# Kernel tuning notes

Measured on AMD Instinct MI355X. Metric: run time of the kernel, lower is better.

Reference implementation:

```python
import jax, jax.numpy as jnp
import numpy as np

B, C, H, W = 2, 64, 96, 96
CI = C // 2  # inter_channels


def _conv1x1(x, w, b):
    # x: (B,C,H,W), w: (O,C), b: (O,) -> (B,O,H,W)
    return jnp.einsum('bchw,oc->bohw', x, w) + b[None, :, None, None]


def setup_inputs() -> dict:
    key = jax.random.key(0)
    ks = jax.random.split(key, 9)
    s_in = 1.0 / np.sqrt(C)
    s_ci = 1.0 / np.sqrt(CI)
    return {
        'x': jax.random.normal(ks[0], (B, C, H, W), jnp.float32),
        'theta_w': jax.random.uniform(ks[1], (CI, C), jnp.float32, -s_in, s_in),
        'theta_b': jax.random.uniform(ks[2], (CI,), jnp.float32, -s_in, s_in),
        'phi_w': jax.random.uniform(ks[3], (CI, C), jnp.float32, -s_in, s_in),
        'phi_b': jax.random.uniform(ks[4], (CI,), jnp.float32, -s_in, s_in),
        'g_w': jax.random.uniform(ks[5], (CI, C), jnp.float32, -s_in, s_in),
        'g_b': jax.random.uniform(ks[6], (CI,), jnp.float32, -s_in, s_in),
        'rec_w': jax.random.uniform(ks[7], (C, CI), jnp.float32, -s_ci, s_ci),
        'rec_b': jax.random.uniform(ks[8], (C,), jnp.float32, -s_ci, s_ci),
    }


def reference(x, theta_w, theta_b, phi_w, phi_b, g_w, g_b, rec_w, rec_b):
    b, c, h, w = x.shape
    n = h * w
    # 1x1 conv projections, flattened to (B, N, CI)
    theta = _conv1x1(x, theta_w, theta_b).reshape(b, CI, n).transpose(0, 2, 1)
    phi = _conv1x1(x, phi_w, phi_b).reshape(b, CI, n)            # (B, CI, N)
    g = _conv1x1(x, g_w, g_b).reshape(b, CI, n).transpose(0, 2, 1)  # (B, N, CI)
    # f = theta @ phi^T / N  (no softmax)
    f = jnp.einsum('bnc,bcm->bnm', theta, phi) / n  # (B, N, N)
    y = jnp.einsum('bnm,bmc->bnc', f, g)            # (B, N, CI)
    y = y.transpose(0, 2, 1).reshape(b, CI, h, w)
    z = x + _conv1x1(y, rec_w, rec_b)
    return z
```

## Files before the change

kernel.cpp:

```cpp
#include <hip/hip_runtime.h>

#define BB 2
#define CC 64
#define CI 32
#define NPIX 9216
#define CH 128
#define NCHK (NPIX / CH)
#define NB (BB * NCHK)
#define SLOT (CI * CI)

__global__ __launch_bounds__(1024) void k1_Mpart(
    const float* __restrict__ x, const float* __restrict__ pw,
    const float* __restrict__ pb, const float* __restrict__ gw,
    const float* __restrict__ gb, float* __restrict__ Mpart) {
  __shared__ float xt[CC][CH + 4];
  __shared__ float pgw[2 * CI][CC + 1];
  __shared__ float Ps[CI][CH + 4];
  __shared__ float Gs[CI][CH + 4];
  const int t = threadIdx.x;
  const int blk = blockIdx.x;
  const int batch = blk / NCHK;
  const int chk = blk - batch * NCHK;
  const float* __restrict__ X = x + (size_t)batch * CC * NPIX + chk * CH;

#pragma unroll
  for (int h = 0; h < 2; ++h) {
    const int idx = t + 1024 * h;
    const int c = idx >> 5;
    const int p4 = (idx & 31) * 4;
    *reinterpret_cast<float4*>(&xt[c][p4]) =
        *reinterpret_cast<const float4*>(&X[(size_t)c * NPIX + p4]);
  }
#pragma unroll
  for (int h = 0; h < 2; ++h) {
    const int idx = t + 1024 * h;
    const int k = idx >> 6, c = idx & 63;
    pgw[k][c] = pw[idx];
    pgw[CI + k][c] = gw[idx];
  }
  __syncthreads();

  {
    const int k = t & 31;
    const int p0 = (t >> 5) * 4;
    float pa[4] = {};
    float ga[4] = {};
    for (int c = 0; c < CC; ++c) {
      const float4 xv = *reinterpret_cast<const float4*>(&xt[c][p0]);
      const float pv = pgw[k][c];
      const float gv = pgw[CI + k][c];
      pa[0] += pv * xv.x; pa[1] += pv * xv.y;
      pa[2] += pv * xv.z; pa[3] += pv * xv.w;
      ga[0] += gv * xv.x; ga[1] += gv * xv.y;
      ga[2] += gv * xv.z; ga[3] += gv * xv.w;
    }
    const float pbk = pb[k];
    const float gbk = gb[k];
    *reinterpret_cast<float4*>(&Ps[k][p0]) =
        make_float4(pa[0] + pbk, pa[1] + pbk, pa[2] + pbk, pa[3] + pbk);
    *reinterpret_cast<float4*>(&Gs[k][p0]) =
        make_float4(ga[0] + gbk, ga[1] + gbk, ga[2] + gbk, ga[3] + gbk);
  }
  __syncthreads();

  {
    const int kk = t >> 5;
    const int l = t & 31;
    float m = 0.f;
    for (int p4 = 0; p4 < CH; p4 += 4) {
      const float4 pv = *reinterpret_cast<const float4*>(&Ps[kk][p4]);
      const float4 gv = *reinterpret_cast<const float4*>(&Gs[l][p4]);
      m += pv.x * gv.x + pv.y * gv.y + pv.z * gv.z + pv.w * gv.w;
    }
    Mpart[(size_t)blk * SLOT + t] = m;
  }
}

__global__ __launch_bounds__(1024) void k2_apply(
    const float* __restrict__ x, const float* __restrict__ tw,
    const float* __restrict__ tb, const float* __restrict__ rw,
    const float* __restrict__ rb, const float* __restrict__ Mpart,
    float* __restrict__ z) {
  __shared__ float xt[CC][CH + 4];
  __shared__ float Ms[CI][CI + 1];
  __shared__ float T1[CI][CC + 2];
  __shared__ float Wt[CC][CC + 2];
  __shared__ float t2[CI];
  __shared__ float bl[CC];
  const int t = threadIdx.x;
  const int blk = blockIdx.x;
  const int batch = blk / NCHK;
  const int chk = blk - batch * NCHK;

#pragma unroll
  for (int h = 0; h < 2; ++h) {
    const int idx = t + 1024 * h;
    const int c = idx >> 5;
    const int p4 = (idx & 31) * 4;
    *reinterpret_cast<float4*>(&xt[c][p4]) = *reinterpret_cast<const float4*>(
        &x[(size_t)batch * CC * NPIX + (size_t)c * NPIX + chk * CH + p4]);
  }

  {
    const float* __restrict__ Mp = Mpart + (size_t)batch * NCHK * SLOT + t;
    float s = 0.f;
#pragma unroll 8
    for (int k = 0; k < NCHK; ++k) s += Mp[(size_t)k * SLOT];
    Ms[t >> 5][t & 31] = s;
  }
  __syncthreads();

  {
#pragma unroll
    for (int q = 0; q < 2; ++q) {
      const int idx = t + 1024 * q;
      const int c = idx >> 6, j = idx & 63;
      float s = 0.f;
      for (int k = 0; k < CI; ++k) s += Ms[k][c] * tw[k * CC + j];
      T1[c][j] = s;
    }
    if (t < CI) {
      float s = 0.f;
      for (int k = 0; k < CI; ++k) s += Ms[k][t] * tb[k];
      t2[t] = s;
    }
  }
  __syncthreads();

  {
    const float invN = 1.0f / (float)NPIX;
#pragma unroll
    for (int q = 0; q < 4; ++q) {
      const int idx = t + 1024 * q;
      const int o = idx >> 6, j = idx & 63;
      float s = 0.f;
      for (int c = 0; c < CI; ++c) s += rw[o * CI + c] * T1[c][j];
      Wt[j][o] = s * invN;
    }
    if (t < CC) {
      float s = 0.f;
      for (int c = 0; c < CI; ++c) s += rw[t * CI + c] * t2[c];
      bl[t] = s * invN + rb[t];
    }
  }
  __syncthreads();

  {
    const int n0 = chk * CH;
    float* __restrict__ Z = z + (size_t)batch * CC * NPIX;
    const int c0 = (t >> 7) * 8;
    const int m0 = t & 127;
    float acc[8] = {};
#pragma unroll 8
    for (int k = 0; k < CC; ++k) {
      const float xv = xt[k][m0];
      const float4 w0 = *reinterpret_cast<const float4*>(&Wt[k][c0]);
      const float4 w1 = *reinterpret_cast<const float4*>(&Wt[k][c0 + 4]);
      acc[0] += w0.x * xv; acc[1] += w0.y * xv;
      acc[2] += w0.z * xv; acc[3] += w0.w * xv;
      acc[4] += w1.x * xv; acc[5] += w1.y * xv;
      acc[6] += w1.z * xv; acc[7] += w1.w * xv;
    }
#pragma unroll
    for (int cc = 0; cc < 8; ++cc) {
      const int c = c0 + cc;
      Z[(size_t)c * NPIX + n0 + m0] = acc[cc] + xt[c][m0] + bl[c];
    }
  }
}

extern "C" void kernel_launch(void* const* d_in, const int* in_sizes, int n_in,
                              void* d_out, int out_size, void* d_ws,
                              size_t ws_size, hipStream_t stream) {
  (void)in_sizes; (void)n_in; (void)out_size; (void)ws_size;
  const float* x  = (const float*)d_in[0];
  const float* tw = (const float*)d_in[1];
  const float* tb = (const float*)d_in[2];
  const float* pw = (const float*)d_in[3];
  const float* pb = (const float*)d_in[4];
  const float* gw = (const float*)d_in[5];
  const float* gb = (const float*)d_in[6];
  const float* rw = (const float*)d_in[7];
  const float* rb = (const float*)d_in[8];
  float* z = (float*)d_out;

  float* Mpart = (float*)d_ws;

  hipLaunchKernelGGL(k1_Mpart, dim3(NB), dim3(1024), 0, stream,
                     x, pw, pb, gw, gb, Mpart);
  hipLaunchKernelGGL(k2_apply, dim3(NB), dim3(1024), 0, stream,
                     x, tw, tb, rw, rb, Mpart, z);
}
```

Measured before the change: 32.07 us.

## Register-tile all compute phases and halve block size to 512 threads

Both kernels drop from 1024 to 512 threads per block. Each compute phase (the projections, the partial M product, T1/Wt construction and the output GEMM) is rewritten so that a subset of threads computes register tiles of 4x8 or 8x8 outputs, loading operands with float4. This cuts shared-memory load traffic per FMA and idle lanes. In exchange, only 64 to 256 threads are active in several phases, which lowers parallelism and latency hiding and raises register pressure.

```diff
diff --git a/kernel.cpp b/kernel.cpp
--- a/kernel.cpp
+++ b/kernel.cpp
@@ -9,12 +9,12 @@
 #define NB (BB * NCHK)
 #define SLOT (CI * CI)
 
-__global__ __launch_bounds__(1024) void k1_Mpart(
+__global__ __launch_bounds__(512) void k1_Mpart(
     const float* __restrict__ x, const float* __restrict__ pw,
     const float* __restrict__ pb, const float* __restrict__ gw,
     const float* __restrict__ gb, float* __restrict__ Mpart) {
   __shared__ float xt[CC][CH + 4];
-  __shared__ float pgw[2 * CI][CC + 1];
+  __shared__ float pgw[2 * CI][CC + 4];
   __shared__ float Ps[CI][CH + 4];
   __shared__ float Gs[CI][CH + 4];
   const int t = threadIdx.x;
@@ -24,8 +24,8 @@
   const float* __restrict__ X = x + (size_t)batch * CC * NPIX + chk * CH;
 
 #pragma unroll
-  for (int h = 0; h < 2; ++h) {
-    const int idx = t + 1024 * h;
+  for (int h = 0; h < 4; ++h) {
+    const int idx = t + 512 * h;
     const int c = idx >> 5;
     const int p4 = (idx & 31) * 4;
     *reinterpret_cast<float4*>(&xt[c][p4]) =
@@ -33,58 +33,91 @@
   }
 #pragma unroll
   for (int h = 0; h < 2; ++h) {
-    const int idx = t + 1024 * h;
-    const int k = idx >> 6, c = idx & 63;
-    pgw[k][c] = pw[idx];
-    pgw[CI + k][c] = gw[idx];
-  }
-  __syncthreads();
-
-  {
-    const int k = t & 31;
-    const int p0 = (t >> 5) * 4;
-    float pa[4] = {};
-    float ga[4] = {};
-    for (int c = 0; c < CC; ++c) {
-      const float4 xv = *reinterpret_cast<const float4*>(&xt[c][p0]);
-      const float pv = pgw[k][c];
-      const float gv = pgw[CI + k][c];
-      pa[0] += pv * xv.x; pa[1] += pv * xv.y;
-      pa[2] += pv * xv.z; pa[3] += pv * xv.w;
-      ga[0] += gv * xv.x; ga[1] += gv * xv.y;
-      ga[2] += gv * xv.z; ga[3] += gv * xv.w;
-    }
-    const float pbk = pb[k];
-    const float gbk = gb[k];
-    *reinterpret_cast<float4*>(&Ps[k][p0]) =
-        make_float4(pa[0] + pbk, pa[1] + pbk, pa[2] + pbk, pa[3] + pbk);
-    *reinterpret_cast<float4*>(&Gs[k][p0]) =
-        make_float4(ga[0] + gbk, ga[1] + gbk, ga[2] + gbk, ga[3] + gbk);
-  }
-  __syncthreads();
-
-  {
-    const int kk = t >> 5;
-    const int l = t & 31;
-    float m = 0.f;
+    const int idx = t + 512 * h;
+    const int r = idx >> 4;
+    const int c4 = (idx & 15) * 4;
+    const float* src = (r < CI) ? &pw[r * CC + c4] : &gw[(r - CI) * CC + c4];
+    *reinterpret_cast<float4*>(&pgw[r][c4]) =
+        *reinterpret_cast<const float4*>(src);
+  }
+  __syncthreads();
+
+  if (t < 128) {
+    const int k0 = (t >> 4) * 4;
+    const int p0 = (t & 15) * 8;
+    float pa[4][8] = {};
+    float ga[4][8] = {};
+    for (int c4 = 0; c4 < CC; c4 += 4) {
+      float4 wp[4], wg[4];
+#pragma unroll
+      for (int i = 0; i < 4; ++i) {
+        wp[i] = *reinterpret_cast<const float4*>(&pgw[k0 + i][c4]);
+        wg[i] = *reinterpret_cast<const float4*>(&pgw[CI + k0 + i][c4]);
+      }
+#pragma unroll
+      for (int j = 0; j < 4; ++j) {
+        const float4 xa = *reinterpret_cast<const float4*>(&xt[c4 + j][p0]);
+        const float4 xb =
+            *reinterpret_cast<const float4*>(&xt[c4 + j][p0 + 4]);
+        const float xv[8] = {xa.x, xa.y, xa.z, xa.w, xb.x, xb.y, xb.z, xb.w};
+#pragma unroll
+        for (int i = 0; i < 4; ++i) {
+          const float wpv = (&wp[i].x)[j];
+          const float wgv = (&wg[i].x)[j];
+#pragma unroll
+          for (int p = 0; p < 8; ++p) {
+            pa[i][p] += wpv * xv[p];
+            ga[i][p] += wgv * xv[p];
+          }
+        }
+      }
+    }
+#pragma unroll
+    for (int i = 0; i < 4; ++i) {
+      const float pbk = pb[k0 + i];
+      const float gbk = gb[k0 + i];
+      *reinterpret_cast<float4*>(&Ps[k0 + i][p0]) = make_float4(
+          pa[i][0] + pbk, pa[i][1] + pbk, pa[i][2] + pbk, pa[i][3] + pbk);
+      *reinterpret_cast<float4*>(&Ps[k0 + i][p0 + 4]) = make_float4(
+          pa[i][4] + pbk, pa[i][5] + pbk, pa[i][6] + pbk, pa[i][7] + pbk);
+      *reinterpret_cast<float4*>(&Gs[k0 + i][p0]) = make_float4(
+          ga[i][0] + gbk, ga[i][1] + gbk, ga[i][2] + gbk, ga[i][3] + gbk);
+      *reinterpret_cast<float4*>(&Gs[k0 + i][p0 + 4]) = make_float4(
+          ga[i][4] + gbk, ga[i][5] + gbk, ga[i][6] + gbk, ga[i][7] + gbk);
+    }
+  }
+  __syncthreads();
+
+  if (t < 256) {
+    const int kk0 = (t >> 4) * 2;
+    const int l0 = (t & 15) * 2;
+    float m[2][2] = {};
     for (int p4 = 0; p4 < CH; p4 += 4) {
-      const float4 pv = *reinterpret_cast<const float4*>(&Ps[kk][p4]);
-      const float4 gv = *reinterpret_cast<const float4*>(&Gs[l][p4]);
-      m += pv.x * gv.x + pv.y * gv.y + pv.z * gv.z + pv.w * gv.w;
-    }
-    Mpart[(size_t)blk * SLOT + t] = m;
+      const float4 pv0 = *reinterpret_cast<const float4*>(&Ps[kk0][p4]);
+      const float4 pv1 = *reinterpret_cast<const float4*>(&Ps[kk0 + 1][p4]);
+      const float4 g0 = *reinterpret_cast<const float4*>(&Gs[l0][p4]);
+      const float4 g1 = *reinterpret_cast<const float4*>(&Gs[l0 + 1][p4]);
+      m[0][0] += pv0.x * g0.x + pv0.y * g0.y + pv0.z * g0.z + pv0.w * g0.w;
+      m[0][1] += pv0.x * g1.x + pv0.y * g1.y + pv0.z * g1.z + pv0.w * g1.w;
+      m[1][0] += pv1.x * g0.x + pv1.y * g0.y + pv1.z * g0.z + pv1.w * g0.w;
+      m[1][1] += pv1.x * g1.x + pv1.y * g1.y + pv1.z * g1.z + pv1.w * g1.w;
+    }
+    float* Mp = Mpart + (size_t)blk * SLOT;
+    *reinterpret_cast<float2*>(&Mp[kk0 * CI + l0]) = make_float2(m[0][0], m[0][1]);
+    *reinterpret_cast<float2*>(&Mp[(kk0 + 1) * CI + l0]) =
+        make_float2(m[1][0], m[1][1]);
   }
 }
 
-__global__ __launch_bounds__(1024) void k2_apply(
+__global__ __launch_bounds__(512) void k2_apply(
     const float* __restrict__ x, const float* __restrict__ tw,
     const float* __restrict__ tb, const float* __restrict__ rw,
     const float* __restrict__ rb, const float* __restrict__ Mpart,
     float* __restrict__ z) {
   __shared__ float xt[CC][CH + 4];
-  __shared__ float Ms[CI][CI + 1];
-  __shared__ float T1[CI][CC + 2];
-  __shared__ float Wt[CC][CC + 2];
+  __shared__ float Wt[CC][CC + 4];
+  __shared__ float T1[CI][CC + 4];
+  __shared__ float Ms[CI][CI + 4];
   __shared__ float t2[CI];
   __shared__ float bl[CC];
   const int t = threadIdx.x;
@@ -93,8 +126,8 @@
   const int chk = blk - batch * NCHK;
 
 #pragma unroll
-  for (int h = 0; h < 2; ++h) {
-    const int idx = t + 1024 * h;
+  for (int h = 0; h < 4; ++h) {
+    const int idx = t + 512 * h;
     const int c = idx >> 5;
     const int p4 = (idx & 31) * 4;
     *reinterpret_cast<float4*>(&xt[c][p4]) = *reinterpret_cast<const float4*>(
@@ -102,69 +135,119 @@
   }
 
   {
-    const float* __restrict__ Mp = Mpart + (size_t)batch * NCHK * SLOT + t;
+    const float* __restrict__ Mp = Mpart + (size_t)batch * NCHK * SLOT;
+    float s0 = 0.f, s1 = 0.f;
+#pragma unroll 8
+    for (int k = 0; k < NCHK; ++k) {
+      s0 += Mp[(size_t)k * SLOT + t];
+      s1 += Mp[(size_t)k * SLOT + t + 512];
+    }
+    Ms[t >> 5][t & 31] = s0;
+    Ms[(t + 512) >> 5][(t + 512) & 31] = s1;
+  }
+  __syncthreads();
+
+  if (t < 64) {
+    const int c0 = (t >> 3) * 4;
+    const int jo = (t & 7) * 8;
+    float a[4][8] = {};
+    for (int k = 0; k < CI; ++k) {
+      const float4 mv = *reinterpret_cast<const float4*>(&Ms[k][c0]);
+      const float4 w0 = *reinterpret_cast<const float4*>(&tw[k * CC + jo]);
+      const float4 w1 = *reinterpret_cast<const float4*>(&tw[k * CC + jo + 4]);
+      const float wv[8] = {w0.x, w0.y, w0.z, w0.w, w1.x, w1.y, w1.z, w1.w};
+      const float mva[4] = {mv.x, mv.y, mv.z, mv.w};
+#pragma unroll
+      for (int ci = 0; ci < 4; ++ci)
+#pragma unroll
+        for (int j = 0; j < 8; ++j) a[ci][j] += mva[ci] * wv[j];
+    }
+#pragma unroll
+    for (int ci = 0; ci < 4; ++ci) {
+      *reinterpret_cast<float4*>(&T1[c0 + ci][jo]) =
+          make_float4(a[ci][0], a[ci][1], a[ci][2], a[ci][3]);
+      *reinterpret_cast<float4*>(&T1[c0 + ci][jo + 4]) =
+          make_float4(a[ci][4], a[ci][5], a[ci][6], a[ci][7]);
+    }
+  } else if (t < 96) {
+    const int c = t - 64;
     float s = 0.f;
-#pragma unroll 8
-    for (int k = 0; k < NCHK; ++k) s += Mp[(size_t)k * SLOT];
-    Ms[t >> 5][t & 31] = s;
-  }
-  __syncthreads();
-
-  {
-#pragma unroll
-    for (int q = 0; q < 2; ++q) {
-      const int idx = t + 1024 * q;
-      const int c = idx >> 6, j = idx & 63;
-      float s = 0.f;
-      for (int k = 0; k < CI; ++k) s += Ms[k][c] * tw[k * CC + j];
-      T1[c][j] = s;
-    }
-    if (t < CI) {
-      float s = 0.f;
-      for (int k = 0; k < CI; ++k) s += Ms[k][t] * tb[k];
-      t2[t] = s;
-    }
-  }
-  __syncthreads();
-
-  {
+    for (int k = 0; k < CI; ++k) s += Ms[k][c] * tb[k];
+    t2[c] = s;
+  }
+  __syncthreads();
+
+  if (t < 64) {
+    const int og = (t >> 3) * 8;
+    const int jo = (t & 7) * 8;
+    float a[8][8] = {};
+    for (int c4 = 0; c4 < CI; c4 += 4) {
+      float4 rv[8];
+#pragma unroll
+      for (int oi = 0; oi < 8; ++oi)
+        rv[oi] = *reinterpret_cast<const float4*>(&rw[(og + oi) * CI + c4]);
+#pragma unroll
+      for (int cj = 0; cj < 4; ++cj) {
+        const float4 t0 = *reinterpret_cast<const float4*>(&T1[c4 + cj][jo]);
+        const float4 t1 =
+            *reinterpret_cast<const float4*>(&T1[c4 + cj][jo + 4]);
+        const float tv[8] = {t0.x, t0.y, t0.z, t0.w, t1.x, t1.y, t1.z, t1.w};
+#pragma unroll
+        for (int oi = 0; oi < 8; ++oi) {
+          const float rvv = (&rv[oi].x)[cj];
+#pragma unroll
+          for (int j = 0; j < 8; ++j) a[oi][j] += rvv * tv[j];
+        }
+      }
+    }
     const float invN = 1.0f / (float)NPIX;
 #pragma unroll
-    for (int q = 0; q < 4; ++q) {
-      const int idx = t + 1024 * q;
-      const int o = idx >> 6, j = idx & 63;
-      float s = 0.f;
-      for (int c = 0; c < CI; ++c) s += rw[o * CI + c] * T1[c][j];
-      Wt[j][o] = s * invN;
-    }
-    if (t < CC) {
-      float s = 0.f;
-      for (int c = 0; c < CI; ++c) s += rw[t * CI + c] * t2[c];
-      bl[t] = s * invN + rb[t];
-    }
-  }
-  __syncthreads();
-
-  {
+    for (int j = 0; j < 8; ++j) {
+      *reinterpret_cast<float4*>(&Wt[jo + j][og]) =
+          make_float4(a[0][j] * invN, a[1][j] * invN, a[2][j] * invN,
+                      a[3][j] * invN);
+      *reinterpret_cast<float4*>(&Wt[jo + j][og + 4]) =
+          make_float4(a[4][j] * invN, a[5][j] * invN, a[6][j] * invN,
+                      a[7][j] * invN);
+    }
+  } else if (t < 128) {
+    const int o = t - 64;
+    float s = 0.f;
+    for (int c = 0; c < CI; ++c) s += rw[o * CI + c] * t2[c];
+    bl[o] = s * (1.0f / (float)NPIX) + rb[o];
+  }
+  __syncthreads();
+
+  if (t < 128) {
+    const int c0 = (t >> 4) * 8;
+    const int p0 = (t & 15) * 8;
     const int n0 = chk * CH;
     float* __restrict__ Z = z + (size_t)batch * CC * NPIX;
-    const int c0 = (t >> 7) * 8;
-    const int m0 = t & 127;
-    float acc[8] = {};
-#pragma unroll 8
+    float acc[8][8] = {};
     for (int k = 0; k < CC; ++k) {
-      const float xv = xt[k][m0];
+      const float4 xa = *reinterpret_cast<const float4*>(&xt[k][p0]);
+      const float4 xb = *reinterpret_cast<const float4*>(&xt[k][p0 + 4]);
       const float4 w0 = *reinterpret_cast<const float4*>(&Wt[k][c0]);
       const float4 w1 = *reinterpret_cast<const float4*>(&Wt[k][c0 + 4]);
-      acc[0] += w0.x * xv; acc[1] += w0.y * xv;
-      acc[2] += w0.z * xv; acc[3] += w0.w * xv;
-      acc[4] += w1.x * xv; acc[5] += w1.y * xv;
-      acc[6] += w1.z * xv; acc[7] += w1.w * xv;
-    }
-#pragma unroll
-    for (int cc = 0; cc < 8; ++cc) {
-      const int c = c0 + cc;
-      Z[(size_t)c * NPIX + n0 + m0] = acc[cc] + xt[c][m0] + bl[c];
+      const float xv[8] = {xa.x, xa.y, xa.z, xa.w, xb.x, xb.y, xb.z, xb.w};
+      const float wv[8] = {w0.x, w0.y, w0.z, w0.w, w1.x, w1.y, w1.z, w1.w};
+#pragma unroll
+      for (int oi = 0; oi < 8; ++oi)
+#pragma unroll
+        for (int p = 0; p < 8; ++p) acc[oi][p] += wv[oi] * xv[p];
+    }
+#pragma unroll
+    for (int oi = 0; oi < 8; ++oi) {
+      const int c = c0 + oi;
+      const float bb2 = bl[c];
+      const float4 xa = *reinterpret_cast<const float4*>(&xt[c][p0]);
+      const float4 xb = *reinterpret_cast<const float4*>(&xt[c][p0 + 4]);
+      *reinterpret_cast<float4*>(&Z[(size_t)c * NPIX + n0 + p0]) =
+          make_float4(acc[oi][0] + xa.x + bb2, acc[oi][1] + xa.y + bb2,
+                      acc[oi][2] + xa.z + bb2, acc[oi][3] + xa.w + bb2);
+      *reinterpret_cast<float4*>(&Z[(size_t)c * NPIX + n0 + p0 + 4]) =
+          make_float4(acc[oi][4] + xb.x + bb2, acc[oi][5] + xb.y + bb2,
+                      acc[oi][6] + xb.z + bb2, acc[oi][7] + xb.w + bb2);
     }
   }
 }
@@ -186,8 +269,8 @@
 
   float* Mpart = (float*)d_ws;
 
-  hipLaunchKernelGGL(k1_Mpart, dim3(NB), dim3(1024), 0, stream,
+  hipLaunchKernelGGL(k1_Mpart, dim3(NB), dim3(512), 0, stream,
                      x, pw, pb, gw, gb, Mpart);
-  hipLaunchKernelGGL(k2_apply, dim3(NB), dim3(1024), 0, stream,
+  hipLaunchKernelGGL(k2_apply, dim3(NB), dim3(512), 0, stream,
                      x, tw, tb, rw, rb, Mpart, z);
 }
```

After: 34.59 us. 1.08x slower.
